# Performance work log

Hardware: AMD Instinct MI355X
Metric: run time of the kernel (lower is better)

Reference implementation:

```python
import jax, jax.numpy as jnp
import numpy as np

TOP_K = 2
CAPACITY_FACTOR = 1.0


def setup_inputs() -> dict:
    key = jax.random.key(0)
    ks = jax.random.split(key, 4)
    S, M, E, V = 32768, 512, 64, 2048
    return {
        "x": jax.random.normal(ks[0], (S, M), jnp.float32),
        "wg": jax.random.normal(ks[1], (E, M), jnp.float32) * (1.0 / np.sqrt(M)),
        "fc1_w": jax.random.normal(ks[2], (E, M, V), jnp.float32) * (1.0 / np.sqrt(M)),
        "fc1_b": jnp.zeros((E, V), jnp.float32),
        "fc2_w": jax.random.normal(ks[3], (E, V, M), jnp.float32) * (1.0 / np.sqrt(V)),
        "fc2_b": jnp.zeros((E, M), jnp.float32),
    }


def _moe_forward(x, wg, fc1_w, fc1_b, fc2_w, fc2_b):
    S, M = x.shape
    E = wg.shape[0]
    K = TOP_K
    # capacity = top_k * int(cap_factor * ceil(S / E))  (static, from shapes)
    C = K * int(CAPACITY_FACTOR * ((S + E - 1) // E))

    # --- gating ---
    logits = x @ wg.T                                    # [S, E]
    gates = jax.nn.softmax(logits, axis=-1)              # [S, E]
    topk_idx = jax.lax.top_k(logits, K)[1]               # [S, K] int32
    masks = jax.nn.one_hot(topk_idx, E, dtype=logits.dtype)  # [S, K, E]
    gates_s = jnp.einsum('se,ske->sk', gates, masks)     # [S, K]

    # load-balance aux loss (fp32 path of load_balance)
    me = gates.sum(axis=0)                               # [E]
    ce = masks[:, 0, :].sum(axis=0)                      # [E]
    l_loss = jnp.sum(me * ce) * (E / (S * S))

    # --- cumsum capacity locations with per-k offsets (acc_base) ---
    counts = masks.sum(axis=0)                           # [K, E]
    prev_counts = jnp.concatenate(
        [jnp.zeros((1, E), logits.dtype), jnp.cumsum(counts, axis=0)[:-1]], axis=0)
    cums = jnp.cumsum(masks, axis=0) - 1.0               # fast_cumsum_sub_one per k
    locs = jnp.einsum('ske,ske->sk', cums + prev_counts[None], masks).astype(jnp.int32)

    # normalize top-k gates (top_k > 1 branch)
    denom = jnp.maximum(gates_s.sum(axis=1, keepdims=True),
                        jnp.finfo(gates_s.dtype).eps)
    gates_n = gates_s / denom                            # [S, K]

    # --- encode: scatter tokens into [E, C, M], overflow tokens dropped ---
    valid = locs < C                                     # [S, K]
    flat_pos = jnp.where(valid, topk_idx.astype(jnp.int32) * C + locs, E * C)
    src = jnp.broadcast_to(x[:, None, :], (S, K, M)).reshape(-1, M)
    disp = jnp.zeros((E * C + 1, M), x.dtype).at[flat_pos.reshape(-1)].add(src)
    disp = disp[:E * C].reshape(E, C, M)                 # world_size=1: AllToAll = id

    # --- fused FFN experts: relu(x @ fc1 + b1) @ fc2 + b2 ---
    h = jax.nn.relu(jnp.einsum('ecm,emv->ecv', disp, fc1_w) + fc1_b[:, None, :])
    eout = jnp.einsum('ecv,evm->ecm', h, fc2_w) + fc2_b[:, None, :]

    # --- decode/combine: gather expert slots, weight by normalized gates ---
    eflat = jnp.concatenate([eout.reshape(E * C, M),
                             jnp.zeros((1, M), eout.dtype)], axis=0)
    gathered = eflat[flat_pos]                           # [S, K, M]
    y = jnp.einsum('sk,skm->sm', gates_n * valid.astype(gates_n.dtype), gathered)
    return y, l_loss


def reference(x, wg, fc1_w, fc1_b, fc2_w, fc2_b):
    return _moe_forward(x, wg, fc1_w, fc1_b, fc2_w, fc2_b)
```

## Files before the change

kernel.cpp:

```cpp
#include <hip/hip_runtime.h>
#include <hip/hip_bf16.h>
#include <stdint.h>

#define S_TOK 32768
#define M_DIM 512
#define E_NUM 64
#define V_DIM 2048
#define CAP   1024

typedef __attribute__((ext_vector_type(8))) short short8;
typedef __attribute__((ext_vector_type(4))) float f32x4;

__device__ __forceinline__ unsigned short f2bf(float f) {
  unsigned int u = __float_as_uint(f);
  unsigned int r = (u + 0x7fffu + ((u >> 16) & 1u)) >> 16;
  return (unsigned short)r;
}
__device__ __forceinline__ float bf2f(unsigned short h) {
  return __uint_as_float(((unsigned int)h) << 16);
}

__device__ __forceinline__ void gload16(const void* g, void* lds) {
  __builtin_amdgcn_global_load_lds(
      (const __attribute__((address_space(1))) void*)g,
      (__attribute__((address_space(3))) void*)lds, 16, 0, 0);
}

__global__ __launch_bounds__(256) void transpose_convert2(const float* __restrict__ w1,
                                                          unsigned short* __restrict__ o1,
                                                          const float* __restrict__ w2,
                                                          unsigned short* __restrict__ o2) {
  __shared__ float ts[64][65];
  int which = blockIdx.z;
  int R = which ? V_DIM : M_DIM;
  int Cc = which ? M_DIM : V_DIM;
  int nbx = Cc / 64;
  int b = blockIdx.y;
  const float* ip = (which ? w2 : w1) + (size_t)b * R * Cc;
  unsigned short* op = (which ? o2 : o1) + (size_t)b * R * Cc;
  int t = blockIdx.x;
  int c0 = (t % nbx) * 64, r0 = (t / nbx) * 64;
  int tid = threadIdx.x;
  int lrow = tid >> 4;
  int lc4 = (tid & 15) * 4;
  #pragma unroll
  for (int i = 0; i < 4; ++i) {
    int row = i * 16 + lrow;
    float4 v = *reinterpret_cast<const float4*>(&ip[(size_t)(r0 + row) * Cc + c0 + lc4]);
    ts[row][lc4 + 0] = v.x; ts[row][lc4 + 1] = v.y;
    ts[row][lc4 + 2] = v.z; ts[row][lc4 + 3] = v.w;
  }
  __syncthreads();
  #pragma unroll
  for (int i = 0; i < 2; ++i) {
    int chunk = i * 256 + tid;
    int c = chunk >> 3;
    int rg = (chunk & 7) * 8;
    short8 o;
    #pragma unroll
    for (int j = 0; j < 8; ++j) o[j] = (short)f2bf(ts[rg + j][c]);
    *reinterpret_cast<short8*>(&op[(size_t)(c0 + c) * R + r0 + rg]) = o;
  }
}

__global__ __launch_bounds__(256) void gating_kernel(
    const float* __restrict__ x, const float* __restrict__ wg,
    int* __restrict__ topk, float* __restrict__ gates_n,
    float* __restrict__ me_part, int* __restrict__ ce_part,
    unsigned short* __restrict__ xbf) {
  __shared__ float4 xs4[16 * 128];
  __shared__ float mered[4][64];
  __shared__ int cered[4][64];
  int tid = threadIdx.x;
  int l = tid & 63, w = tid >> 6;
  int tb = blockIdx.x * 16;
  const float4* xg4 = reinterpret_cast<const float4*>(x) + (size_t)tb * 128;
  ushort4* xb4 = reinterpret_cast<ushort4*>(xbf) + (size_t)tb * 128;
  #pragma unroll
  for (int i = 0; i < 8; ++i) {
    float4 v = xg4[i * 256 + tid];
    xs4[i * 256 + tid] = v;
    ushort4 o;
    o.x = f2bf(v.x); o.y = f2bf(v.y); o.z = f2bf(v.z); o.w = f2bf(v.w);
    xb4[i * 256 + tid] = o;
  }
  __syncthreads();

  const float4* wg4 = reinterpret_cast<const float4*>(wg) + (size_t)l * 128;
  float acc[4] = {0.f, 0.f, 0.f, 0.f};
  for (int i = 0; i < 128; ++i) {
    float4 wv = wg4[i];
    #pragma unroll
    for (int t = 0; t < 4; ++t) {
      float4 xv = xs4[(w * 4 + t) * 128 + i];
      acc[t] += xv.x * wv.x; acc[t] += xv.y * wv.y;
      acc[t] += xv.z * wv.z; acc[t] += xv.w * wv.w;
    }
  }

  float melocal = 0.f;
  int celocal = 0;
  for (int t = 0; t < 4; ++t) {
    float v = acc[t];
    float bv = v; int bi = l;
    #pragma unroll
    for (int off = 32; off; off >>= 1) {
      float ov = __shfl_xor(bv, off);
      int oi = __shfl_xor(bi, off);
      if (ov > bv || (ov == bv && oi < bi)) { bv = ov; bi = oi; }
    }
    float v2 = (l == bi) ? -INFINITY : v;
    float bv2 = v2; int bi2 = l;
    #pragma unroll
    for (int off = 32; off; off >>= 1) {
      float ov = __shfl_xor(bv2, off);
      int oi = __shfl_xor(bi2, off);
      if (ov > bv2 || (ov == bv2 && oi < bi2)) { bv2 = ov; bi2 = oi; }
    }
    float ex = expf(v - bv);
    float s = ex;
    #pragma unroll
    for (int off = 32; off; off >>= 1) s += __shfl_xor(s, off);
    melocal += ex / s;
    if (l == bi) celocal += 1;
    if (l == 0) {
      int sidx = tb + w * 4 + t;
      topk[sidx * 2 + 0] = bi;
      topk[sidx * 2 + 1] = bi2;
      float g1 = 1.0f / s;
      float g2 = expf(bv2 - bv) / s;
      float denom = fmaxf(g1 + g2, 1.1920929e-07f);
      gates_n[sidx * 2 + 0] = g1 / denom;
      gates_n[sidx * 2 + 1] = g2 / denom;
    }
  }
  mered[w][l] = melocal;
  cered[w][l] = celocal;
  __syncthreads();
  if (tid < 64) {
    me_part[blockIdx.x * 64 + tid] =
        mered[0][tid] + mered[1][tid] + mered[2][tid] + mered[3][tid];
    ce_part[blockIdx.x * 64 + tid] =
        cered[0][tid] + cered[1][tid] + cered[2][tid] + cered[3][tid];
  }
}

__global__ __launch_bounds__(256) void rank_kernel(const int* __restrict__ topk,
                                                   int* __restrict__ dest,
                                                   int* __restrict__ slot_map) {
  int e = blockIdx.x;
  int tid = threadIdx.x;
  int l = tid & 63, w = tid >> 6;
  int4 minus1 = {-1, -1, -1, -1};
  reinterpret_cast<int4*>(slot_map + e * CAP)[tid] = minus1;

  const int2* tk = reinterpret_cast<const int2*>(topk);
  int base = tid * 128;
  int c0 = 0, c1 = 0;
  for (int j = 0; j < 128; ++j) {
    int2 p = tk[base + j];
    c0 += (p.x == e); c1 += (p.y == e);
  }
  int i0 = c0, i1 = c1;
  #pragma unroll
  for (int off = 1; off < 64; off <<= 1) {
    int t0 = __shfl_up(i0, off);
    int t1 = __shfl_up(i1, off);
    if (l >= off) { i0 += t0; i1 += t1; }
  }
  __shared__ int ws0[4], ws1[4], wo0[4], wo1[4], tot0s;
  if (l == 63) { ws0[w] = i0; ws1[w] = i1; }
  __syncthreads();
  if (tid == 0) {
    int a = 0, b = 0;
    #pragma unroll
    for (int j = 0; j < 4; ++j) { wo0[j] = a; a += ws0[j]; wo1[j] = b; b += ws1[j]; }
    tot0s = a;
  }
  __syncthreads();
  int loc0 = wo0[w] + i0 - c0;
  int loc1 = tot0s + wo1[w] + i1 - c1;
  for (int j = 0; j < 128; ++j) {
    int s = base + j;
    int2 p = tk[s];
    if (p.x == e) {
      int d = (loc0 < CAP) ? e * CAP + loc0 : -1;
      dest[s * 2] = d;
      if (d >= 0) slot_map[d] = s;
      loc0++;
    }
    if (p.y == e) {
      int d = (loc1 < CAP) ? e * CAP + loc1 : -1;
      dest[s * 2 + 1] = d;
      if (d >= 0) slot_map[d] = s;
      loc1++;
    }
  }
}

#define PH_TOP                                                                 \
  __builtin_amdgcn_sched_barrier(0);                                           \
  __builtin_amdgcn_s_barrier();                                                \
  asm volatile("s_waitcnt lgkmcnt(0)" ::: "memory");                           \
  __builtin_amdgcn_sched_barrier(0);                                           \
  __builtin_amdgcn_s_setprio(1);
#define PH_BOT                                                                 \
  __builtin_amdgcn_s_setprio(0);                                               \
  __builtin_amdgcn_sched_barrier(0);                                           \
  __builtin_amdgcn_s_barrier();

struct SmemGemm {
  union {
    struct {
      unsigned short A[2][256 * 64];
      unsigned short B[2][256 * 64];
    } st;
    unsigned short C[256 * 258];
  };
};

template <int KD, int ND, int NBX, int NBY, int NLOOPN, bool GATHER, bool RELU>
__global__ __launch_bounds__(512, 2) void gemm8_kernel(
    const unsigned short* __restrict__ A,
    const unsigned short* __restrict__ BT,
    const float* __restrict__ bias,
    const int* __restrict__ slot_map,
    unsigned short* __restrict__ out) {
  constexpr int NT = KD / 64;
  constexpr int NBXG = NBX / NLOOPN;
  __shared__ SmemGemm sm;

  const int tid = threadIdx.x;
  const int l = tid & 63;
  const int w = tid >> 6;
  const int wm = w >> 2;
  const int wn = w & 3;
  const int lr = l & 15;
  const int lk8 = l >> 4;

  const int nwg = E_NUM * NBXG * NBY;
  const int cpx = nwg >> 3;
  int lid = ((int)blockIdx.x % 8) * cpx + (int)blockIdx.x / 8;
  const int e = lid / (NBXG * NBY);
  int rem = lid % (NBXG * NBY);
  const int n0base = (rem / NBY) * (NLOOPN * 256);
  const int r0 = (rem % NBY) * 256;

  const int cg8 = (((l & 7) ^ (l >> 3)) * 8);

  int arows[2][2], brows[2][2];
  uint32_t offA[2][2], ldsA[2][2], ldsB[2][2];
  #pragma unroll
  for (int sel = 0; sel < 2; ++sel) {
    #pragma unroll
    for (int i = 0; i < 2; ++i) {
      int lr128 = i * 64 + w * 8 + (l >> 3);
      int ar = ((lr128 >> 6) * 128) + sel * 64 + (lr128 & 63);
      int br = ((lr128 >> 5) * 64) + sel * 32 + (lr128 & 31);
      arows[sel][i] = ar;
      brows[sel][i] = br;
      ldsA[sel][i] = ar * 64 + (l & 7) * 8;
      ldsB[sel][i] = br * 64 + (l & 7) * 8;
      int arow;
      if (GATHER) {
        int s = slot_map[e * CAP + r0 + ar];
        if (s < 0) s = 0;
        arow = s;
      } else {
        arow = e * CAP + r0 + ar;
      }
      offA[sel][i] = (uint32_t)arow * KD + cg8;
    }
  }
  const unsigned short* Bexp = BT + (size_t)e * ND * KD;

  const int sg0 = ((0 + lk8) ^ (lr & 7)) * 8;
  const int sg1 = ((4 + lk8) ^ (lr & 7)) * 8;

#define STAGE_A(sel, p, kt)                                                    \
  do {                                                                         \
    gload16(A + offA[sel][0] + (kt) * 64, &sm.st.A[p][ldsA[sel][0]]);          \
    gload16(A + offA[sel][1] + (kt) * 64, &sm.st.A[p][ldsA[sel][1]]);          \
  } while (0)
#define STAGE_B(sel, p, kt)                                                    \
  do {                                                                         \
    gload16(Bexp + offB[sel][0] + (kt) * 64, &sm.st.B[p][ldsB[sel][0]]);       \
    gload16(Bexp + offB[sel][1] + (kt) * 64, &sm.st.B[p][ldsB[sel][1]]);       \
  } while (0)
#define RD_A(p, mh, mi, ks)                                                    \
  (*reinterpret_cast<const short8*>(                                           \
      &sm.st.A[p][(wm * 128 + (mh) * 64 + (mi) * 16 + lr) * 64 + ((ks) ? sg1 : sg0)]))
#define RD_B(p, nh, ni, ks)                                                    \
  (*reinterpret_cast<const short8*>(                                           \
      &sm.st.B[p][(wn * 64 + (nh) * 32 + (ni) * 16 + lr) * 64 + ((ks) ? sg1 : sg0)]))

  short8 afr[2][4][2];
  short8 bfr[2][2];
  f32x4 acc[8][4];
  f32x4 zero = {0.f, 0.f, 0.f, 0.f};

  for (int it = 0; it < NLOOPN; ++it) {
    const int n0 = n0base + it * 256;
    uint32_t offB[2][2];
    #pragma unroll
    for (int sel = 0; sel < 2; ++sel)
      #pragma unroll
      for (int i = 0; i < 2; ++i)
        offB[sel][i] = (uint32_t)(n0 + brows[sel][i]) * KD + cg8;

    #pragma unroll
    for (int m = 0; m < 8; ++m)
      #pragma unroll
      for (int n = 0; n < 4; ++n) acc[m][n] = zero;

    STAGE_A(0, 0, 0); STAGE_A(1, 0, 0); STAGE_B(0, 0, 0); STAGE_B(1, 0, 0);
    STAGE_A(0, 1, 1); STAGE_A(1, 1, 1); STAGE_B(0, 1, 1);
    asm volatile("s_waitcnt vmcnt(6)" ::: "memory");
    __builtin_amdgcn_sched_barrier(0);
    __builtin_amdgcn_s_barrier();

#define GROUP(k, p)                                                            \
  {                                                                            \
               \
    _Pragma("unroll") for (int mi = 0; mi < 4; ++mi) {                         \
      afr[0][mi][0] = RD_A(p, 0, mi, 0);                                       \
      afr[0][mi][1] = RD_A(p, 0, mi, 1);                                       \
    }                                                                          \
    _Pragma("unroll") for (int ni = 0; ni < 2; ++ni) {                         \
      bfr[ni][0] = RD_B(p, 0, ni, 0);                                          \
      bfr[ni][1] = RD_B(p, 0, ni, 1);                                          \
    }                                                                          \
    if ((k) + 1 < NT) { STAGE_B(1, (p) ^ 1, (k) + 1); }                        \
    PH_TOP                                                                     \
    _Pragma("unroll") for (int mi = 0; mi < 4; ++mi)                           \
      _Pragma("unroll") for (int ni = 0; ni < 2; ++ni) {                       \
        acc[mi][ni] = __builtin_amdgcn_mfma_f32_16x16x32_bf16(                 \
            afr[0][mi][0], bfr[ni][0], acc[mi][ni], 0, 0, 0);                  \
        acc[mi][ni] = __builtin_amdgcn_mfma_f32_16x16x32_bf16(                 \
            afr[0][mi][1], bfr[ni][1], acc[mi][ni], 0, 0, 0);                  \
      }                                                                        \
    PH_BOT                                                                     \
                 \
    _Pragma("unroll") for (int mi = 0; mi < 4; ++mi) {                         \
      afr[1][mi][0] = RD_A(p, 1, mi, 0);                                       \
      afr[1][mi][1] = RD_A(p, 1, mi, 1);                                       \
    }                                                                          \
    if ((k) + 2 < NT) { STAGE_A(0, p, (k) + 2); }                              \
    PH_TOP                                                                     \
    _Pragma("unroll") for (int mi = 0; mi < 4; ++mi)                           \
      _Pragma("unroll") for (int ni = 0; ni < 2; ++ni) {                       \
        acc[4 + mi][ni] = __builtin_amdgcn_mfma_f32_16x16x32_bf16(             \
            afr[1][mi][0], bfr[ni][0], acc[4 + mi][ni], 0, 0, 0);              \
        acc[4 + mi][ni] = __builtin_amdgcn_mfma_f32_16x16x32_bf16(             \
            afr[1][mi][1], bfr[ni][1], acc[4 + mi][ni], 0, 0, 0);              \
      }                                                                        \
    PH_BOT                                                                     \
                 \
    _Pragma("unroll") for (int ni = 0; ni < 2; ++ni) {                         \
      bfr[ni][0] = RD_B(p, 1, ni, 0);                                          \
      bfr[ni][1] = RD_B(p, 1, ni, 1);                                          \
    }                                                                          \
    if ((k) + 2 < NT) { STAGE_A(1, p, (k) + 2); }                              \
    PH_TOP                                                                     \
    _Pragma("unroll") for (int mi = 0; mi < 4; ++mi)                           \
      _Pragma("unroll") for (int ni = 0; ni < 2; ++ni) {                       \
        acc[mi][2 + ni] = __builtin_amdgcn_mfma_f32_16x16x32_bf16(             \
            afr[0][mi][0], bfr[ni][0], acc[mi][2 + ni], 0, 0, 0);              \
        acc[mi][2 + ni] = __builtin_amdgcn_mfma_f32_16x16x32_bf16(             \
            afr[0][mi][1], bfr[ni][1], acc[mi][2 + ni], 0, 0, 0);              \
      }                                                                        \
    PH_BOT                                                                     \
             \
    if ((k) + 2 < NT) { STAGE_B(0, p, (k) + 2); }                              \
    __builtin_amdgcn_sched_barrier(0);                                         \
    __builtin_amdgcn_s_barrier();                                              \
    __builtin_amdgcn_s_setprio(1);                                             \
    _Pragma("unroll") for (int mi = 0; mi < 4; ++mi)                           \
      _Pragma("unroll") for (int ni = 0; ni < 2; ++ni) {                       \
        acc[4 + mi][2 + ni] = __builtin_amdgcn_mfma_f32_16x16x32_bf16(         \
            afr[1][mi][0], bfr[ni][0], acc[4 + mi][2 + ni], 0, 0, 0);          \
        acc[4 + mi][2 + ni] = __builtin_amdgcn_mfma_f32_16x16x32_bf16(         \
            afr[1][mi][1], bfr[ni][1], acc[4 + mi][2 + ni], 0, 0, 0);          \
      }                                                                        \
    __builtin_amdgcn_s_setprio(0);                                             \
    __builtin_amdgcn_sched_barrier(0);                                         \
    if ((k) + 2 < NT) {                                                        \
      asm volatile("s_waitcnt vmcnt(6)" ::: "memory");                         \
    } else {                                                                   \
      asm volatile("s_waitcnt vmcnt(0)" ::: "memory");                         \
    }                                                                          \
    __builtin_amdgcn_sched_barrier(0);                                         \
    __builtin_amdgcn_s_barrier();                                              \
  }

    for (int kk = 0; kk < NT / 2; ++kk) {
      int k0 = 2 * kk;
      GROUP(k0, 0)
      GROUP(k0 + 1, 1)
    }
#undef GROUP

    #pragma unroll
    for (int n = 0; n < 4; ++n) {
      int gcl = wn * 64 + n * 16 + lr;
      float bv = bias[e * ND + n0 + gcl];
      #pragma unroll
      for (int m = 0; m < 8; ++m) {
        int trow = wm * 128 + m * 16 + lk8 * 4;
        #pragma unroll
        for (int j = 0; j < 4; ++j) {
          float v = acc[m][n][j] + bv;
          if (RELU) v = fmaxf(v, 0.f);
          sm.C[(trow + j) * 258 + gcl] = f2bf(v);
        }
      }
    }
    __syncthreads();
    #pragma unroll
    for (int i = 0; i < 16; ++i) {
      int chunk = i * 512 + tid;
      int row = chunk >> 5;
      int c8 = chunk & 31;
      short8 v = *reinterpret_cast<const short8*>(&sm.C[row * 258 + c8 * 8]);
      *reinterpret_cast<short8*>(
          &out[((size_t)(e * CAP + r0 + row)) * ND + n0 + c8 * 8]) = v;
    }
    if (it + 1 < NLOOPN) {
      asm volatile("s_waitcnt vmcnt(0)" ::: "memory");
      __syncthreads();
    }
  }
#undef STAGE_A
#undef STAGE_B
#undef RD_A
#undef RD_B
}

__global__ __launch_bounds__(256) void decode_kernel(
    const unsigned short* __restrict__ Y, const int* __restrict__ dest,
    const float* __restrict__ gn, float* __restrict__ y,
    const float* __restrict__ me_part, const int* __restrict__ ce_part,
    float* __restrict__ loss_out) {
  int tid = threadIdx.x;
  if (blockIdx.x == gridDim.x - 1) {
    int e = tid & 63, ch = tid >> 6;
    float sme = 0.f, sce = 0.f;
    for (int j = 0; j < 512; ++j) {
      int idx = (ch * 512 + j) * 64 + e;
      sme += me_part[idx];
      sce += (float)ce_part[idx];
    }
    __shared__ float redm[4][64];
    __shared__ float redc[4][64];
    redm[ch][e] = sme;
    redc[ch][e] = sce;
    __syncthreads();
    if (tid < 64) {
      float m = redm[0][tid] + redm[1][tid] + redm[2][tid] + redm[3][tid];
      float c = redc[0][tid] + redc[1][tid] + redc[2][tid] + redc[3][tid];
      float p = m * c;
      #pragma unroll
      for (int off = 32; off; off >>= 1) p += __shfl_xor(p, off);
      if (tid == 0) loss_out[0] = p * ((float)E_NUM / ((float)S_TOK * (float)S_TOK));
    }
    return;
  }
  int t = blockIdx.x * 4 + (tid >> 6);
  int m0 = (tid & 63) * 8;
  int d0 = dest[t * 2 + 0], d1 = dest[t * 2 + 1];
  float g0 = gn[t * 2 + 0], g1 = gn[t * 2 + 1];
  float o[8];
  #pragma unroll
  for (int j = 0; j < 8; ++j) o[j] = 0.f;
  if (d0 >= 0) {
    short8 v = *reinterpret_cast<const short8*>(&Y[(size_t)d0 * M_DIM + m0]);
    #pragma unroll
    for (int j = 0; j < 8; ++j) o[j] += g0 * bf2f((unsigned short)v[j]);
  }
  if (d1 >= 0) {
    short8 v = *reinterpret_cast<const short8*>(&Y[(size_t)d1 * M_DIM + m0]);
    #pragma unroll
    for (int j = 0; j < 8; ++j) o[j] += g1 * bf2f((unsigned short)v[j]);
  }
  float4 o0 = {o[0], o[1], o[2], o[3]};
  float4 o1 = {o[4], o[5], o[6], o[7]};
  *reinterpret_cast<float4*>(&y[(size_t)t * M_DIM + m0]) = o0;
  *reinterpret_cast<float4*>(&y[(size_t)t * M_DIM + m0 + 4]) = o1;
}

extern "C" void kernel_launch(void* const* d_in, const int* in_sizes, int n_in,
                              void* d_out, int out_size, void* d_ws, size_t ws_size,
                              hipStream_t stream) {
  const float* x     = (const float*)d_in[0];
  const float* wg    = (const float*)d_in[1];
  const float* fc1_w = (const float*)d_in[2];
  const float* fc1_b = (const float*)d_in[3];
  const float* fc2_w = (const float*)d_in[4];
  const float* fc2_b = (const float*)d_in[5];
  float* y = (float*)d_out;
  float* loss_out = y + (size_t)S_TOK * M_DIM;

  char* ws = (char*)d_ws;
  size_t off = 0;
  auto alloc = [&](size_t bytes) {
    char* p = ws + off;
    off += (bytes + 255) & ~(size_t)255;
    return p;
  };
  unsigned short* wT1 = (unsigned short*)alloc((size_t)E_NUM * V_DIM * M_DIM * 2);
  unsigned short* wT2 = (unsigned short*)alloc((size_t)E_NUM * M_DIM * V_DIM * 2);
  unsigned short* H   = (unsigned short*)alloc((size_t)E_NUM * CAP * V_DIM * 2);
  unsigned short* xbf = (unsigned short*)alloc((size_t)S_TOK * M_DIM * 2);
  int*   topk     = (int*)alloc((size_t)S_TOK * 2 * 4);
  float* gatesn   = (float*)alloc((size_t)S_TOK * 2 * 4);
  int*   dest     = (int*)alloc((size_t)S_TOK * 2 * 4);
  int*   slot_map = (int*)alloc((size_t)E_NUM * CAP * 4);
  float* me_part  = (float*)alloc((size_t)(S_TOK / 16) * 64 * 4);
  int*   ce_part  = (int*)alloc((size_t)(S_TOK / 16) * 64 * 4);
  unsigned short* Y = wT1;

  transpose_convert2<<<dim3(256, E_NUM, 2), 256, 0, stream>>>(fc1_w, wT1, fc2_w, wT2);

  gating_kernel<<<S_TOK / 16, 256, 0, stream>>>(x, wg, topk, gatesn, me_part, ce_part, xbf);
  rank_kernel<<<E_NUM, 256, 0, stream>>>(topk, dest, slot_map);

  gemm8_kernel<512, 2048, 8, 4, 4, true, true>
      <<<E_NUM * 2 * 4, 512, 0, stream>>>(xbf, wT1, fc1_b, slot_map, H);
  gemm8_kernel<2048, 512, 2, 4, 1, false, false>
      <<<E_NUM * 2 * 4, 512, 0, stream>>>(H, wT2, fc2_b, slot_map, Y);

  decode_kernel<<<S_TOK / 4 + 1, 256, 0, stream>>>(Y, dest, gatesn, y,
                                                   me_part, ce_part, loss_out);
}
```

Before: 873.4 us.

## Merge gating and weight transpose into one kernel; drop N-loop in fc1 GEMM

Fuses the weight transpose/convert and gating kernels into a single prep launch, with block ranges dispatching to either task and a shared-memory union, so the two independent jobs can run concurrently on the GPU. The fc1 GEMM no longer loops over four N tiles per workgroup; it launches four times as many workgroups (2048 instead of 512), each computing one 256x256 tile. This trades per-block A-tile reuse across N for more parallelism and fewer serialized epilogues. The larger launch may refetch the A rows more often.

```diff
diff --git a/kernel.cpp b/kernel.cpp
--- a/kernel.cpp
+++ b/kernel.cpp
@@ -26,52 +26,66 @@
       (__attribute__((address_space(3))) void*)lds, 16, 0, 0);
 }
 
-__global__ __launch_bounds__(256) void transpose_convert2(const float* __restrict__ w1,
-                                                          unsigned short* __restrict__ o1,
-                                                          const float* __restrict__ w2,
-                                                          unsigned short* __restrict__ o2) {
-  __shared__ float ts[64][65];
-  int which = blockIdx.z;
-  int R = which ? V_DIM : M_DIM;
-  int Cc = which ? M_DIM : V_DIM;
-  int nbx = Cc / 64;
-  int b = blockIdx.y;
-  const float* ip = (which ? w2 : w1) + (size_t)b * R * Cc;
-  unsigned short* op = (which ? o2 : o1) + (size_t)b * R * Cc;
-  int t = blockIdx.x;
-  int c0 = (t % nbx) * 64, r0 = (t / nbx) * 64;
-  int tid = threadIdx.x;
-  int lrow = tid >> 4;
-  int lc4 = (tid & 15) * 4;
-  #pragma unroll
-  for (int i = 0; i < 4; ++i) {
-    int row = i * 16 + lrow;
-    float4 v = *reinterpret_cast<const float4*>(&ip[(size_t)(r0 + row) * Cc + c0 + lc4]);
-    ts[row][lc4 + 0] = v.x; ts[row][lc4 + 1] = v.y;
-    ts[row][lc4 + 2] = v.z; ts[row][lc4 + 3] = v.w;
-  }
-  __syncthreads();
-  #pragma unroll
-  for (int i = 0; i < 2; ++i) {
-    int chunk = i * 256 + tid;
-    int c = chunk >> 3;
-    int rg = (chunk & 7) * 8;
-    short8 o;
-    #pragma unroll
-    for (int j = 0; j < 8; ++j) o[j] = (short)f2bf(ts[rg + j][c]);
-    *reinterpret_cast<short8*>(&op[(size_t)(c0 + c) * R + r0 + rg]) = o;
-  }
-}
-
-__global__ __launch_bounds__(256) void gating_kernel(
+#define GATE_BLKS (S_TOK / 16)
+#define TR_TILES_PER (M_DIM / 64) * (V_DIM / 64)
+
+struct PrepSmem {
+  union {
+    struct {
+      float4 xs4[16 * 128];
+      float mered[4][64];
+      int cered[4][64];
+    } g;
+    float ts[64][65];
+  };
+};
+
+__global__ __launch_bounds__(256) void prep_kernel(
     const float* __restrict__ x, const float* __restrict__ wg,
     int* __restrict__ topk, float* __restrict__ gates_n,
     float* __restrict__ me_part, int* __restrict__ ce_part,
-    unsigned short* __restrict__ xbf) {
-  __shared__ float4 xs4[16 * 128];
-  __shared__ float mered[4][64];
-  __shared__ int cered[4][64];
+    unsigned short* __restrict__ xbf,
+    const float* __restrict__ w1, unsigned short* __restrict__ o1,
+    const float* __restrict__ w2, unsigned short* __restrict__ o2) {
+  __shared__ PrepSmem sm;
   int tid = threadIdx.x;
+
+  if (blockIdx.x >= GATE_BLKS) {
+    int t = blockIdx.x - GATE_BLKS;
+    int which = t >> 14;
+    t &= 16383;
+    int R = which ? V_DIM : M_DIM;
+    int Cc = which ? M_DIM : V_DIM;
+    int nbx = Cc / 64;
+    int tilesPer = (R / 64) * nbx;
+    int b = t / tilesPer;
+    int tt = t % tilesPer;
+    const float* ip = (which ? w2 : w1) + (size_t)b * R * Cc;
+    unsigned short* op = (which ? o2 : o1) + (size_t)b * R * Cc;
+    int c0 = (tt % nbx) * 64, r0 = (tt / nbx) * 64;
+    int lrow = tid >> 4;
+    int lc4 = (tid & 15) * 4;
+    #pragma unroll
+    for (int i = 0; i < 4; ++i) {
+      int row = i * 16 + lrow;
+      float4 v = *reinterpret_cast<const float4*>(&ip[(size_t)(r0 + row) * Cc + c0 + lc4]);
+      sm.ts[row][lc4 + 0] = v.x; sm.ts[row][lc4 + 1] = v.y;
+      sm.ts[row][lc4 + 2] = v.z; sm.ts[row][lc4 + 3] = v.w;
+    }
+    __syncthreads();
+    #pragma unroll
+    for (int i = 0; i < 2; ++i) {
+      int chunk = i * 256 + tid;
+      int c = chunk >> 3;
+      int rg = (chunk & 7) * 8;
+      short8 o;
+      #pragma unroll
+      for (int j = 0; j < 8; ++j) o[j] = (short)f2bf(sm.ts[rg + j][c]);
+      *reinterpret_cast<short8*>(&op[(size_t)(c0 + c) * R + r0 + rg]) = o;
+    }
+    return;
+  }
+
   int l = tid & 63, w = tid >> 6;
   int tb = blockIdx.x * 16;
   const float4* xg4 = reinterpret_cast<const float4*>(x) + (size_t)tb * 128;
@@ -79,7 +93,7 @@
   #pragma unroll
   for (int i = 0; i < 8; ++i) {
     float4 v = xg4[i * 256 + tid];
-    xs4[i * 256 + tid] = v;
+    sm.g.xs4[i * 256 + tid] = v;
     ushort4 o;
     o.x = f2bf(v.x); o.y = f2bf(v.y); o.z = f2bf(v.z); o.w = f2bf(v.w);
     xb4[i * 256 + tid] = o;
@@ -92,7 +106,7 @@
     float4 wv = wg4[i];
     #pragma unroll
     for (int t = 0; t < 4; ++t) {
-      float4 xv = xs4[(w * 4 + t) * 128 + i];
+      float4 xv = sm.g.xs4[(w * 4 + t) * 128 + i];
       acc[t] += xv.x * wv.x; acc[t] += xv.y * wv.y;
       acc[t] += xv.z * wv.z; acc[t] += xv.w * wv.w;
     }
@@ -134,14 +148,14 @@
       gates_n[sidx * 2 + 1] = g2 / denom;
     }
   }
-  mered[w][l] = melocal;
-  cered[w][l] = celocal;
+  sm.g.mered[w][l] = melocal;
+  sm.g.cered[w][l] = celocal;
   __syncthreads();
   if (tid < 64) {
     me_part[blockIdx.x * 64 + tid] =
-        mered[0][tid] + mered[1][tid] + mered[2][tid] + mered[3][tid];
+        sm.g.mered[0][tid] + sm.g.mered[1][tid] + sm.g.mered[2][tid] + sm.g.mered[3][tid];
     ce_part[blockIdx.x * 64 + tid] =
-        cered[0][tid] + cered[1][tid] + cered[2][tid] + cered[3][tid];
+        sm.g.cered[0][tid] + sm.g.cered[1][tid] + sm.g.cered[2][tid] + sm.g.cered[3][tid];
   }
 }
 
@@ -219,7 +233,7 @@
   };
 };
 
-template <int KD, int ND, int NBX, int NBY, int NLOOPN, bool GATHER, bool RELU>
+template <int KD, int ND, int NBX, int NBY, bool GATHER, bool RELU>
 __global__ __launch_bounds__(512, 2) void gemm8_kernel(
     const unsigned short* __restrict__ A,
     const unsigned short* __restrict__ BT,
@@ -227,7 +241,6 @@
     const int* __restrict__ slot_map,
     unsigned short* __restrict__ out) {
   constexpr int NT = KD / 64;
-  constexpr int NBXG = NBX / NLOOPN;
   __shared__ SmemGemm sm;
 
   const int tid = threadIdx.x;
@@ -238,18 +251,17 @@
   const int lr = l & 15;
   const int lk8 = l >> 4;
 
-  const int nwg = E_NUM * NBXG * NBY;
+  const int nwg = E_NUM * NBX * NBY;
   const int cpx = nwg >> 3;
   int lid = ((int)blockIdx.x % 8) * cpx + (int)blockIdx.x / 8;
-  const int e = lid / (NBXG * NBY);
-  int rem = lid % (NBXG * NBY);
-  const int n0base = (rem / NBY) * (NLOOPN * 256);
+  const int e = lid / (NBX * NBY);
+  int rem = lid % (NBX * NBY);
+  const int n0 = (rem / NBY) * 256;
   const int r0 = (rem % NBY) * 256;
 
   const int cg8 = (((l & 7) ^ (l >> 3)) * 8);
 
-  int arows[2][2], brows[2][2];
-  uint32_t offA[2][2], ldsA[2][2], ldsB[2][2];
+  uint32_t offA[2][2], offB[2][2], ldsA[2][2], ldsB[2][2];
   #pragma unroll
   for (int sel = 0; sel < 2; ++sel) {
     #pragma unroll
@@ -257,8 +269,6 @@
       int lr128 = i * 64 + w * 8 + (l >> 3);
       int ar = ((lr128 >> 6) * 128) + sel * 64 + (lr128 & 63);
       int br = ((lr128 >> 5) * 64) + sel * 32 + (lr128 & 31);
-      arows[sel][i] = ar;
-      brows[sel][i] = br;
       ldsA[sel][i] = ar * 64 + (l & 7) * 8;
       ldsB[sel][i] = br * 64 + (l & 7) * 8;
       int arow;
@@ -270,6 +280,7 @@
         arow = e * CAP + r0 + ar;
       }
       offA[sel][i] = (uint32_t)arow * KD + cg8;
+      offB[sel][i] = (uint32_t)(n0 + br) * KD + cg8;
     }
   }
   const unsigned short* Bexp = BT + (size_t)e * ND * KD;
@@ -298,26 +309,16 @@
   short8 bfr[2][2];
   f32x4 acc[8][4];
   f32x4 zero = {0.f, 0.f, 0.f, 0.f};
-
-  for (int it = 0; it < NLOOPN; ++it) {
-    const int n0 = n0base + it * 256;
-    uint32_t offB[2][2];
-    #pragma unroll
-    for (int sel = 0; sel < 2; ++sel)
-      #pragma unroll
-      for (int i = 0; i < 2; ++i)
-        offB[sel][i] = (uint32_t)(n0 + brows[sel][i]) * KD + cg8;
-
-    #pragma unroll
-    for (int m = 0; m < 8; ++m)
-      #pragma unroll
-      for (int n = 0; n < 4; ++n) acc[m][n] = zero;
-
-    STAGE_A(0, 0, 0); STAGE_A(1, 0, 0); STAGE_B(0, 0, 0); STAGE_B(1, 0, 0);
-    STAGE_A(0, 1, 1); STAGE_A(1, 1, 1); STAGE_B(0, 1, 1);
-    asm volatile("s_waitcnt vmcnt(6)" ::: "memory");
-    __builtin_amdgcn_sched_barrier(0);
-    __builtin_amdgcn_s_barrier();
+  #pragma unroll
+  for (int m = 0; m < 8; ++m)
+    #pragma unroll
+    for (int n = 0; n < 4; ++n) acc[m][n] = zero;
+
+  STAGE_A(0, 0, 0); STAGE_A(1, 0, 0); STAGE_B(0, 0, 0); STAGE_B(1, 0, 0);
+  STAGE_A(0, 1, 1); STAGE_A(1, 1, 1); STAGE_B(0, 1, 1);
+  asm volatile("s_waitcnt vmcnt(6)" ::: "memory");
+  __builtin_amdgcn_sched_barrier(0);
+  __builtin_amdgcn_s_barrier();
 
 #define GROUP(k, p)                                                            \
   {                                                                            \
@@ -393,47 +394,42 @@
     __builtin_amdgcn_s_barrier();                                              \
   }
 
-    for (int kk = 0; kk < NT / 2; ++kk) {
-      int k0 = 2 * kk;
-      GROUP(k0, 0)
-      GROUP(k0 + 1, 1)
-    }
+  for (int kk = 0; kk < NT / 2; ++kk) {
+    int k0 = 2 * kk;
+    GROUP(k0, 0)
+    GROUP(k0 + 1, 1)
+  }
 #undef GROUP
-
-    #pragma unroll
-    for (int n = 0; n < 4; ++n) {
-      int gcl = wn * 64 + n * 16 + lr;
-      float bv = bias[e * ND + n0 + gcl];
-      #pragma unroll
-      for (int m = 0; m < 8; ++m) {
-        int trow = wm * 128 + m * 16 + lk8 * 4;
-        #pragma unroll
-        for (int j = 0; j < 4; ++j) {
-          float v = acc[m][n][j] + bv;
-          if (RELU) v = fmaxf(v, 0.f);
-          sm.C[(trow + j) * 258 + gcl] = f2bf(v);
-        }
-      }
-    }
-    __syncthreads();
-    #pragma unroll
-    for (int i = 0; i < 16; ++i) {
-      int chunk = i * 512 + tid;
-      int row = chunk >> 5;
-      int c8 = chunk & 31;
-      short8 v = *reinterpret_cast<const short8*>(&sm.C[row * 258 + c8 * 8]);
-      *reinterpret_cast<short8*>(
-          &out[((size_t)(e * CAP + r0 + row)) * ND + n0 + c8 * 8]) = v;
-    }
-    if (it + 1 < NLOOPN) {
-      asm volatile("s_waitcnt vmcnt(0)" ::: "memory");
-      __syncthreads();
-    }
-  }
 #undef STAGE_A
 #undef STAGE_B
 #undef RD_A
 #undef RD_B
+
+  #pragma unroll
+  for (int n = 0; n < 4; ++n) {
+    int gcl = wn * 64 + n * 16 + lr;
+    float bv = bias[e * ND + n0 + gcl];
+    #pragma unroll
+    for (int m = 0; m < 8; ++m) {
+      int trow = wm * 128 + m * 16 + lk8 * 4;
+      #pragma unroll
+      for (int j = 0; j < 4; ++j) {
+        float v = acc[m][n][j] + bv;
+        if (RELU) v = fmaxf(v, 0.f);
+        sm.C[(trow + j) * 258 + gcl] = f2bf(v);
+      }
+    }
+  }
+  __syncthreads();
+  #pragma unroll
+  for (int i = 0; i < 16; ++i) {
+    int chunk = i * 512 + tid;
+    int row = chunk >> 5;
+    int c8 = chunk & 31;
+    short8 v = *reinterpret_cast<const short8*>(&sm.C[row * 258 + c8 * 8]);
+    *reinterpret_cast<short8*>(
+        &out[((size_t)(e * CAP + r0 + row)) * ND + n0 + c8 * 8]) = v;
+  }
 }
 
 __global__ __launch_bounds__(256) void decode_kernel(
@@ -519,14 +515,14 @@
   int*   ce_part  = (int*)alloc((size_t)(S_TOK / 16) * 64 * 4);
   unsigned short* Y = wT1;
 
-  transpose_convert2<<<dim3(256, E_NUM, 2), 256, 0, stream>>>(fc1_w, wT1, fc2_w, wT2);
-
-  gating_kernel<<<S_TOK / 16, 256, 0, stream>>>(x, wg, topk, gatesn, me_part, ce_part, xbf);
+  prep_kernel<<<GATE_BLKS + 32768, 256, 0, stream>>>(
+      x, wg, topk, gatesn, me_part, ce_part, xbf, fc1_w, wT1, fc2_w, wT2);
+
   rank_kernel<<<E_NUM, 256, 0, stream>>>(topk, dest, slot_map);
 
-  gemm8_kernel<512, 2048, 8, 4, 4, true, true>
-      <<<E_NUM * 2 * 4, 512, 0, stream>>>(xbf, wT1, fc1_b, slot_map, H);
-  gemm8_kernel<2048, 512, 2, 4, 1, false, false>
+  gemm8_kernel<512, 2048, 8, 4, true, true>
+      <<<E_NUM * 8 * 4, 512, 0, stream>>>(xbf, wT1, fc1_b, slot_map, H);
+  gemm8_kernel<2048, 512, 2, 4, false, false>
       <<<E_NUM * 2 * 4, 512, 0, stream>>>(H, wT2, fc2_b, slot_map, Y);
 
   decode_kernel<<<S_TOK / 4 + 1, 256, 0, stream>>>(Y, dest, gatesn, y,
```

Measured after the change: 767.4 us. 1.14x faster.
